# Kernel tuning notes

Measured on AMD Instinct MI355X. Metric: run time of the kernel, lower is better.

The kernel has to match this reference:

```python
import jax, jax.numpy as jnp
import numpy as np

BITS = 1.58
EPS = 1e-8


def absmean_quantize(w, bits=BITS, scale_method='mean'):
    # gamma over the whole weight tensor (CPU path of original)
    if scale_method == 'mean':
        gamma = jnp.mean(jnp.abs(w))
    else:
        gamma = jnp.max(jnp.abs(w))
    levels = 2.0 ** bits - 1.0  # ~1.989 for 1.58-bit ternary-ish
    half = levels / 2.0
    return jnp.clip(jnp.round(w / (gamma + EPS) * half), -half, half)


def setup_inputs() -> dict:
    key = jax.random.key(0)
    k_x, k_w, k_b = jax.random.split(key, 3)
    B, S, D_IN, D_OUT = 8, 2048, 4096, 4096
    x = jax.random.normal(k_x, (B, S, D_IN), dtype=jnp.float32)
    # kaiming_uniform_(a=sqrt(5)) -> bound = sqrt(6/((1+5)*fan_in)) = 1/sqrt(fan_in)
    bound = 1.0 / np.sqrt(D_IN)
    weight = jax.random.uniform(k_w, (D_OUT, D_IN), minval=-bound, maxval=bound, dtype=jnp.float32)
    bias = jax.random.uniform(k_b, (D_OUT,), minval=-bound, maxval=bound, dtype=jnp.float32)
    return {"x": x, "weight": weight, "bias": bias}


def reference(x, weight, bias):
    qw = absmean_quantize(weight)                      # [D_OUT, D_IN]
    out = jnp.einsum('bsi,oi->bso', x, qw)             # F.linear without bias
    return out + bias
```

## Files before the change

kernel.cpp:

```cpp
#include <hip/hip_runtime.h>
#include <math.h>
#include <stdint.h>


#define MDIM 16384
#define NDIM 4096
#define KDIM 4096

__global__ void absmean_reduce(const float4* __restrict__ w4,
                               double* __restrict__ gsum, int n4) {
  int tid = blockIdx.x * blockDim.x + threadIdx.x;
  int stride = gridDim.x * blockDim.x;
  double s = 0.0;
  for (int i = tid; i < n4; i += stride) {
    float4 v = w4[i];
    s += (double)fabsf(v.x) + (double)fabsf(v.y) +
         (double)fabsf(v.z) + (double)fabsf(v.w);
  }
  for (int off = 32; off > 0; off >>= 1) s += __shfl_down(s, off, 64);
  __shared__ double partial[4];
  int ln = threadIdx.x & 63, wv = threadIdx.x >> 6;
  if (ln == 0) partial[wv] = s;
  __syncthreads();
  if (threadIdx.x == 0) {
    double t = partial[0] + partial[1] + partial[2] + partial[3];
    atomicAdd(gsum, t);
  }
}

__device__ __forceinline__ unsigned short tern_bf16(float w, float g, float h) {
  float q = rintf(w / g * h);
  q = fminf(fmaxf(q, -1.0f), 1.0f);
  return (unsigned short)(__float_as_uint(q) >> 16);
}

__global__ void quantize_w(const float4* __restrict__ w4,
                           const double* __restrict__ gsum,
                           ushort4* __restrict__ wq, int n4, float halfF) {
  const float gamma = (float)(*gsum * (1.0 / 16777216.0)) + 1e-8f;
  int tid = blockIdx.x * blockDim.x + threadIdx.x;
  int stride = gridDim.x * blockDim.x;
  for (int i = tid; i < n4; i += stride) {
    float4 v = w4[i];
    ushort4 o;
    o.x = tern_bf16(v.x, gamma, halfF);
    o.y = tern_bf16(v.y, gamma, halfF);
    o.z = tern_bf16(v.z, gamma, halfF);
    o.w = tern_bf16(v.w, gamma, halfF);
    wq[i] = o;
  }
}

__device__ __forceinline__ unsigned bf16_rne(float f) {
  unsigned u = __float_as_uint(f);
  return (u + 0x7FFFu + ((u >> 16) & 1u)) >> 16;
}
__device__ __forceinline__ unsigned pack2(float lo, float hi) {
  return bf16_rne(lo) | (bf16_rne(hi) << 16);
}

__global__ void cvt_x(const float4* __restrict__ x4, uint4* __restrict__ xb,
                      int n8) {
  int tid = blockIdx.x * blockDim.x + threadIdx.x;
  int stride = gridDim.x * blockDim.x;
  for (int i = tid; i < n8; i += stride) {
    float4 a = x4[2 * i];
    float4 b = x4[2 * i + 1];
    uint4 o;
    o.x = pack2(a.x, a.y);
    o.y = pack2(a.z, a.w);
    o.z = pack2(b.x, b.y);
    o.w = pack2(b.z, b.w);
    xb[i] = o;
  }
}

typedef __attribute__((ext_vector_type(8))) short bf16x8;
typedef __attribute__((ext_vector_type(4))) float f32x4;

#define BM 256
#define BN 256
#define BK 64
#define NTK (KDIM / BK)

__device__ __forceinline__ void async16(const short* g, short* l) {
  __builtin_amdgcn_global_load_lds(
      (const __attribute__((address_space(1))) unsigned int*)g,
      (__attribute__((address_space(3))) unsigned int*)l, 16, 0, 0);
}

__global__ __launch_bounds__(512, 2) void gemm_tern_256(
    const short* __restrict__ A,
    const short* __restrict__ Bw,
    const float* __restrict__ bias,
    float* __restrict__ out,
    float scale) {
  extern __shared__ short lds[];

  const int tid = threadIdx.x;
  const int wv = tid >> 6;
  const int ln = tid & 63;
  const int wr = wv >> 2;
  const int wc = wv & 3;
  const int l15 = ln & 15;
  const int lq = ln >> 4;
  const int l7 = ln & 7;

  const int orig = blockIdx.x;
  const int wg = ((orig & 7) << 7) | (orig >> 3);
  const int bm = (wg >> 4) * BM;
  const int bn = (wg & 15) * BN;

  const int g8 = ln >> 3;
  const int sw = (l7 ^ (g8 & 7)) << 3;
  const int grp0 = wv * 2, grp1 = wv * 2 + 1;
  const short* aP0 = A + (size_t)(bm + grp0 * 8 + g8) * KDIM + sw;
  const short* aP1 = A + (size_t)(bm + grp1 * 8 + g8) * KDIM + sw;
  const short* bP0 = Bw + (size_t)(bn + grp0 * 8 + g8) * KDIM + sw;
  const short* bP1 = Bw + (size_t)(bn + grp1 * 8 + g8) * KDIM + sw;
  const int d0 = grp0 * 512, d1 = grp1 * 512;

  int rowA[4], rowB[2], chk[2];
#pragma unroll
  for (int m = 0; m < 4; ++m) rowA[m] = (wr * 64 + m * 16 + l15) * 64;
#pragma unroll
  for (int n = 0; n < 2; ++n) rowB[n] = (wc * 32 + n * 16 + l15) * 64;
#pragma unroll
  for (int ks = 0; ks < 2; ++ks) chk[ks] = (((ks * 4 + lq) ^ l7) << 3);

  f32x4 acc[2][2][4][2] = {};

#define KOF(s) ((size_t)(((s) < NTK) ? (s) : 0) * BK)
#define STAGE_A(DST, H, S)                              \
  do {                                                  \
    const size_t koA_ = KOF(S) + (size_t)(H) * 128 * KDIM; \
    async16(aP0 + koA_, (DST) + (H) * 8192 + d0);       \
    async16(aP1 + koA_, (DST) + (H) * 8192 + d1);       \
  } while (0)
#define STAGE_B(DST, H, S)                                  \
  do {                                                      \
    const size_t koB_ = KOF(S) + (size_t)(H) * 128 * KDIM;  \
    async16(bP0 + koB_, (DST) + 16384 + (H) * 8192 + d0);   \
    async16(bP1 + koB_, (DST) + 16384 + (H) * 8192 + d1);   \
  } while (0)

  {
    short* b0 = lds;
    short* b1 = lds + 32768;
    STAGE_A(b0, 0, 0);
    STAGE_B(b0, 0, 0);
    STAGE_B(b0, 1, 0);
    STAGE_A(b0, 1, 0);
    STAGE_A(b1, 0, 1);
    STAGE_B(b1, 0, 1);
  }
  asm volatile("s_waitcnt vmcnt(4)" ::: "memory");
  __builtin_amdgcn_sched_barrier(0);
  __builtin_amdgcn_s_barrier();

#define PHASE(MH, NH, STAGE_STMT, POST_STMT)                                  \
  do {                                                                        \
    bf16x8 fa[4][2], fb[2][2];                                                \
    const short* Ah_ = C + (MH) * 8192;                                       \
    const short* Bh_ = C + 16384 + (NH) * 8192;                               \
    _Pragma("unroll") for (int m = 0; m < 4; ++m) {                           \
      fa[m][0] = *(const bf16x8*)(Ah_ + rowA[m] + chk[0]);                    \
      fa[m][1] = *(const bf16x8*)(Ah_ + rowA[m] + chk[1]);                    \
    }                                                                         \
    _Pragma("unroll") for (int n = 0; n < 2; ++n) {                           \
      fb[n][0] = *(const bf16x8*)(Bh_ + rowB[n] + chk[0]);                    \
      fb[n][1] = *(const bf16x8*)(Bh_ + rowB[n] + chk[1]);                    \
    }                                                                         \
    STAGE_STMT;                                                               \
    __builtin_amdgcn_sched_barrier(0);                                        \
    __builtin_amdgcn_s_barrier();                                             \
    asm volatile("s_waitcnt lgkmcnt(0)" ::: "memory");                        \
    __builtin_amdgcn_sched_barrier(0);                                        \
    __builtin_amdgcn_s_setprio(1);                                            \
    _Pragma("unroll") for (int m = 0; m < 4; ++m)                             \
        _Pragma("unroll") for (int n = 0; n < 2; ++n) {                       \
      acc[MH][NH][m][n] = __builtin_amdgcn_mfma_f32_16x16x32_bf16(            \
          fa[m][0], fb[n][0], acc[MH][NH][m][n], 0, 0, 0);                    \
      acc[MH][NH][m][n] = __builtin_amdgcn_mfma_f32_16x16x32_bf16(            \
          fa[m][1], fb[n][1], acc[MH][NH][m][n], 0, 0, 0);                    \
    }                                                                         \
    __builtin_amdgcn_s_setprio(0);                                            \
    POST_STMT;                                                                \
    __builtin_amdgcn_sched_barrier(0);                                        \
    __builtin_amdgcn_s_barrier();                                             \
  } while (0)

  for (int kt = 0; kt < NTK; ++kt) {
    short* C = lds + ((kt & 1) << 15);
    short* Nx = lds + (((kt & 1) ^ 1) << 15);
    PHASE(0, 0, STAGE_B(Nx, 1, kt + 1), ((void)0));
    PHASE(0, 1, STAGE_A(Nx, 1, kt + 1), ((void)0));
    PHASE(1, 0, STAGE_A(C, 0, kt + 2), ((void)0));
    PHASE(1, 1, STAGE_B(C, 0, kt + 2),
          asm volatile("s_waitcnt vmcnt(4)" ::: "memory"));
  }

  const int colb = bn + wc * 32 + l15;
  const int rowb = bm + wr * 64 + (lq << 2);
#pragma unroll
  for (int nh = 0; nh < 2; ++nh)
#pragma unroll
    for (int n = 0; n < 2; ++n) {
      const int col = colb + nh * 128 + n * 16;
      const float bj = bias[col];
#pragma unroll
      for (int mh = 0; mh < 2; ++mh)
#pragma unroll
        for (int m = 0; m < 4; ++m) {
          const int row = rowb + mh * 128 + m * 16;
#pragma unroll
          for (int r = 0; r < 4; ++r)
            out[(size_t)(row + r) * NDIM + col] =
                fmaf(acc[mh][nh][m][n][r], scale, bj);
        }
    }
}

extern "C" void kernel_launch(void* const* d_in, const int* in_sizes, int n_in,
                              void* d_out, int out_size, void* d_ws,
                              size_t ws_size, hipStream_t stream) {
  const float* x = (const float*)d_in[0];
  const float* w = (const float*)d_in[1];
  const float* bias = (const float*)d_in[2];
  float* out = (float*)d_out;

  char* ws = (char*)d_ws;
  double* gsum = (double*)ws;
  short* xb = (short*)(ws + 256);
  short* wq = (short*)(ws + 256 + (size_t)MDIM * KDIM * 2);

  const float kHalfF = (float)((pow(2.0, 1.58) - 1.0) * 0.5);

  static bool attr_done = false;
  if (!attr_done) {
    (void)hipFuncSetAttribute((const void*)gemm_tern_256,
                              hipFuncAttributeMaxDynamicSharedMemorySize,
                              131072);
    attr_done = true;
  }

  hipMemsetAsync(gsum, 0, sizeof(double), stream);

  const int nW4 = (NDIM * KDIM) / 4;
  absmean_reduce<<<1024, 256, 0, stream>>>((const float4*)w, gsum, nW4);

  quantize_w<<<4096, 256, 0, stream>>>((const float4*)w, gsum, (ushort4*)wq,
                                       nW4, kHalfF);

  const int nX8 = (MDIM * KDIM) / 8;
  cvt_x<<<8192, 256, 0, stream>>>((const float4*)x, (uint4*)xb, nX8);

  dim3 grid((MDIM / BM) * (NDIM / BN));
  gemm_tern_256<<<grid, 512, 131072, stream>>>(xb, wq, bias, out, kHalfF);
}
```

Measured before the change: 996.6 us.

## Reuse LDS fragments across MFMA phases via serpentine quadrant order

Keeps the A and B register fragments alive across the four quadrant phases instead of reloading both from LDS in every phase. The phases now run in the order (0,0),(0,1),(1,1),(1,0), so each phase reloads only one operand and the last phase loads nothing. This cuts LDS read traffic per k-step roughly in half. The cost is more live vector registers, since both B fragment sets stay live, and that could reduce occupancy or cause spills.

```diff
diff --git a/kernel.cpp b/kernel.cpp
--- a/kernel.cpp
+++ b/kernel.cpp
@@ -120,28 +120,50 @@
   const short* bP1 = Bw + (size_t)(bn + grp1 * 8 + g8) * KDIM + sw;
   const int d0 = grp0 * 512, d1 = grp1 * 512;
 
-  int rowA[4], rowB[2], chk[2];
-#pragma unroll
-  for (int m = 0; m < 4; ++m) rowA[m] = (wr * 64 + m * 16 + l15) * 64;
-#pragma unroll
-  for (int n = 0; n < 2; ++n) rowB[n] = (wc * 32 + n * 16 + l15) * 64;
-#pragma unroll
-  for (int ks = 0; ks < 2; ++ks) chk[ks] = (((ks * 4 + lq) ^ l7) << 3);
+  const int c0 = (lq ^ l7) << 3;
+  const int c1 = ((4 + lq) ^ l7) << 3;
+  const int aRow = (wr * 64 + l15) * 64;
+  const int bRow = 16384 + (wc * 32 + l15) * 64;
 
   f32x4 acc[2][2][4][2] = {};
+  bf16x8 faA[4][2];
+  bf16x8 fbB0[2][2], fbB1[2][2];
 
 #define KOF(s) ((size_t)(((s) < NTK) ? (s) : 0) * BK)
-#define STAGE_A(DST, H, S)                              \
-  do {                                                  \
+#define STAGE_A(DST, H, S)                                 \
+  do {                                                     \
     const size_t koA_ = KOF(S) + (size_t)(H) * 128 * KDIM; \
-    async16(aP0 + koA_, (DST) + (H) * 8192 + d0);       \
-    async16(aP1 + koA_, (DST) + (H) * 8192 + d1);       \
+    async16(aP0 + koA_, (DST) + (H) * 8192 + d0);          \
+    async16(aP1 + koA_, (DST) + (H) * 8192 + d1);          \
   } while (0)
-#define STAGE_B(DST, H, S)                                  \
-  do {                                                      \
-    const size_t koB_ = KOF(S) + (size_t)(H) * 128 * KDIM;  \
-    async16(bP0 + koB_, (DST) + 16384 + (H) * 8192 + d0);   \
-    async16(bP1 + koB_, (DST) + 16384 + (H) * 8192 + d1);   \
+#define STAGE_B(DST, H, S)                                 \
+  do {                                                     \
+    const size_t koB_ = KOF(S) + (size_t)(H) * 128 * KDIM; \
+    async16(bP0 + koB_, (DST) + 16384 + (H) * 8192 + d0);  \
+    async16(bP1 + koB_, (DST) + 16384 + (H) * 8192 + d1);  \
+  } while (0)
+
+#define SYNC1                                            \
+  __builtin_amdgcn_sched_barrier(0);                     \
+  __builtin_amdgcn_s_barrier();                          \
+  asm volatile("s_waitcnt lgkmcnt(0)" ::: "memory");     \
+  __builtin_amdgcn_sched_barrier(0)
+
+#define SYNC2                                            \
+  __builtin_amdgcn_sched_barrier(0);                     \
+  __builtin_amdgcn_s_barrier()
+
+#define MFMA_QUAD(MH, NH, FB)                                        \
+  do {                                                               \
+    __builtin_amdgcn_s_setprio(1);                                   \
+    _Pragma("unroll") for (int m = 0; m < 4; ++m)                    \
+        _Pragma("unroll") for (int n = 0; n < 2; ++n) {              \
+      acc[MH][NH][m][n] = __builtin_amdgcn_mfma_f32_16x16x32_bf16(   \
+          faA[m][0], FB[n][0], acc[MH][NH][m][n], 0, 0, 0);          \
+      acc[MH][NH][m][n] = __builtin_amdgcn_mfma_f32_16x16x32_bf16(   \
+          faA[m][1], FB[n][1], acc[MH][NH][m][n], 0, 0, 0);          \
+    }                                                                \
+    __builtin_amdgcn_s_setprio(0);                                   \
   } while (0)
 
   {
@@ -158,46 +180,55 @@
   __builtin_amdgcn_sched_barrier(0);
   __builtin_amdgcn_s_barrier();
 
-#define PHASE(MH, NH, STAGE_STMT, POST_STMT)                                  \
-  do {                                                                        \
-    bf16x8 fa[4][2], fb[2][2];                                                \
-    const short* Ah_ = C + (MH) * 8192;                                       \
-    const short* Bh_ = C + 16384 + (NH) * 8192;                               \
-    _Pragma("unroll") for (int m = 0; m < 4; ++m) {                           \
-      fa[m][0] = *(const bf16x8*)(Ah_ + rowA[m] + chk[0]);                    \
-      fa[m][1] = *(const bf16x8*)(Ah_ + rowA[m] + chk[1]);                    \
-    }                                                                         \
-    _Pragma("unroll") for (int n = 0; n < 2; ++n) {                           \
-      fb[n][0] = *(const bf16x8*)(Bh_ + rowB[n] + chk[0]);                    \
-      fb[n][1] = *(const bf16x8*)(Bh_ + rowB[n] + chk[1]);                    \
-    }                                                                         \
-    STAGE_STMT;                                                               \
-    __builtin_amdgcn_sched_barrier(0);                                        \
-    __builtin_amdgcn_s_barrier();                                             \
-    asm volatile("s_waitcnt lgkmcnt(0)" ::: "memory");                        \
-    __builtin_amdgcn_sched_barrier(0);                                        \
-    __builtin_amdgcn_s_setprio(1);                                            \
-    _Pragma("unroll") for (int m = 0; m < 4; ++m)                             \
-        _Pragma("unroll") for (int n = 0; n < 2; ++n) {                       \
-      acc[MH][NH][m][n] = __builtin_amdgcn_mfma_f32_16x16x32_bf16(            \
-          fa[m][0], fb[n][0], acc[MH][NH][m][n], 0, 0, 0);                    \
-      acc[MH][NH][m][n] = __builtin_amdgcn_mfma_f32_16x16x32_bf16(            \
-          fa[m][1], fb[n][1], acc[MH][NH][m][n], 0, 0, 0);                    \
-    }                                                                         \
-    __builtin_amdgcn_s_setprio(0);                                            \
-    POST_STMT;                                                                \
-    __builtin_amdgcn_sched_barrier(0);                                        \
-    __builtin_amdgcn_s_barrier();                                             \
-  } while (0)
-
   for (int kt = 0; kt < NTK; ++kt) {
-    short* C = lds + ((kt & 1) << 15);
-    short* Nx = lds + (((kt & 1) ^ 1) << 15);
-    PHASE(0, 0, STAGE_B(Nx, 1, kt + 1), ((void)0));
-    PHASE(0, 1, STAGE_A(Nx, 1, kt + 1), ((void)0));
-    PHASE(1, 0, STAGE_A(C, 0, kt + 2), ((void)0));
-    PHASE(1, 1, STAGE_B(C, 0, kt + 2),
-          asm volatile("s_waitcnt vmcnt(4)" ::: "memory"));
+    const int curS = (kt & 1) << 15;
+    short* Cb = lds + curS;
+    short* Nx = lds + (curS ^ 32768);
+    const short* a0 = Cb + aRow + c0;
+    const short* a1 = Cb + aRow + c1;
+    const short* b0 = Cb + bRow + c0;
+    const short* b1 = Cb + bRow + c1;
+
+#pragma unroll
+    for (int m = 0; m < 4; ++m) {
+      faA[m][0] = *(const bf16x8*)(a0 + m * 1024);
+      faA[m][1] = *(const bf16x8*)(a1 + m * 1024);
+    }
+#pragma unroll
+    for (int n = 0; n < 2; ++n) {
+      fbB0[n][0] = *(const bf16x8*)(b0 + n * 1024);
+      fbB0[n][1] = *(const bf16x8*)(b1 + n * 1024);
+    }
+    STAGE_B(Nx, 1, kt + 1);
+    SYNC1;
+    MFMA_QUAD(0, 0, fbB0);
+    SYNC2;
+
+#pragma unroll
+    for (int n = 0; n < 2; ++n) {
+      fbB1[n][0] = *(const bf16x8*)(b0 + 8192 + n * 1024);
+      fbB1[n][1] = *(const bf16x8*)(b1 + 8192 + n * 1024);
+    }
+    STAGE_A(Nx, 1, kt + 1);
+    SYNC1;
+    MFMA_QUAD(0, 1, fbB1);
+    SYNC2;
+
+#pragma unroll
+    for (int m = 0; m < 4; ++m) {
+      faA[m][0] = *(const bf16x8*)(a0 + 8192 + m * 1024);
+      faA[m][1] = *(const bf16x8*)(a1 + 8192 + m * 1024);
+    }
+    STAGE_A(Cb, 0, kt + 2);
+    SYNC1;
+    MFMA_QUAD(1, 1, fbB1);
+    SYNC2;
+
+    STAGE_B(Cb, 0, kt + 2);
+    SYNC1;
+    MFMA_QUAD(1, 0, fbB0);
+    asm volatile("s_waitcnt vmcnt(4)" ::: "memory");
+    SYNC2;
   }
 
   const int colb = bn + wc * 32 + l15;
```

Result: faster. 939.6 us (-5.7%).
